# Optimization experiments

Measured on AMD Instinct MI355X. Metric: run time of the kernel, lower is better.

Reference implementation:

```python
import jax, jax.numpy as jnp
import numpy as np

N_TOKENS = 32768
DIM = 2048
N_EXPERTS = 256
N_GROUPS = 8
N_LIMITED_GROUPS = 4
TOP_K = 8
ROUTE_SCALE = 2.5


def setup_inputs() -> dict:
    key = jax.random.key(0)
    k1, k2, k3, k4 = jax.random.split(key, 4)
    x = jax.random.normal(k1, (N_TOKENS, DIM), dtype=jnp.float32)
    w1 = jax.random.normal(k2, (N_EXPERTS, DIM), dtype=jnp.float32) * (DIM ** -0.5)
    b_lin = jax.random.normal(k3, (N_EXPERTS,), dtype=jnp.float32) * 0.02
    bias = jax.random.normal(k4, (N_EXPERTS,), dtype=jnp.float32) * 0.02
    return {"x": x, "w1": w1, "b_lin": b_lin, "bias": bias}


def reference(x, w1, b_lin, bias):
    n = x.shape[0]
    # gate GEMM: [N, dim] x [dim, E] -> [N, E]
    logits = jnp.einsum("nd,ed->ne", x, w1) + b_lin
    # sigmoid scoring with L1 normalization
    s = jax.nn.sigmoid(logits)
    s = s / jnp.sum(s, axis=-1, keepdims=True)
    # routing-correction bias (torch code adds it in place, so it is also in the
    # gathered values via the original_scores alias)
    s = s + bias
    original_scores = s
    # group-limited masking: keep only top n_limited_groups groups (amax score,
    # since use_bias=True)
    g = s.reshape(n, N_GROUPS, N_EXPERTS // N_GROUPS)
    group_scores = jnp.max(g, axis=-1)                      # [N, G]
    _, gidx = jax.lax.top_k(group_scores, N_LIMITED_GROUPS)  # [N, Glim]
    keep = jnp.zeros((n, N_GROUPS), dtype=bool).at[
        jnp.arange(n)[:, None], gidx].set(True)
    masked = jnp.where(keep[:, :, None], g, -jnp.inf).reshape(n, N_EXPERTS)
    # final top-k over masked scores, gather from (bias-added) original scores
    _, indices = jax.lax.top_k(masked, TOP_K)               # [N, k]
    values = jnp.take_along_axis(original_scores, indices, axis=1) * ROUTE_SCALE
    return values.astype(x.dtype), indices
```

## Files before the change

### kernel.cpp

```cpp
#include <hip/hip_runtime.h>
#include <math.h>

#define NTOK   32768
#define DIM    2048
#define NE     256
#define NG     8
#define GSZ    32
#define NLIM   4
#define TOPK   8
#define RSCALE 2.5f
#define TAU    4e-7f

#define BT      64
#define THREADS 256
#define KT      16
#define NKT     (DIM / KT)
#define WOFF    262144
#define TILE_B  16384

typedef __bf16 bf16x8 __attribute__((ext_vector_type(8)));
typedef float  f32x16 __attribute__((ext_vector_type(16)));

typedef const __attribute__((address_space(1))) void GASV;
typedef __attribute__((address_space(3))) void LASV;

__device__ __forceinline__ void gload16(const void* g, void* l) {
    __builtin_amdgcn_global_load_lds((GASV*)g, (LASV*)l, 16, 0, 0);
}

__device__ __forceinline__ void split_pack(float4 a, float4 b,
                                           bf16x8& h8, bf16x8& r8) {
    float v[8] = {a.x, a.y, a.z, a.w, b.x, b.y, b.z, b.w};
    union { unsigned int u[4]; bf16x8 v8; } H, R;
#pragma unroll
    for (int q = 0; q < 4; ++q) {
        const unsigned int u0 = __float_as_uint(v[2 * q]);
        const unsigned int u1 = __float_as_uint(v[2 * q + 1]);
        H.u[q] = (u0 >> 16) | (u1 & 0xFFFF0000u);
        const float r0 = v[2 * q]     - __uint_as_float(u0 & 0xFFFF0000u);
        const float r1 = v[2 * q + 1] - __uint_as_float(u1 & 0xFFFF0000u);
        R.u[q] = (__float_as_uint(r0) >> 16) |
                 (__float_as_uint(r1) & 0xFFFF0000u);
    }
    h8 = H.v8; r8 = R.v8;
}

__global__ __launch_bounds__(256) void wsplit_kernel(
    const float* __restrict__ w1, unsigned int* __restrict__ wt)
{
    const int g  = blockIdx.x * 256 + threadIdx.x;
    const int e  = g & 255;
    const int hi = (g >> 8) & 1;
    const int p  = (g >> 9) & 1;
    const int kt = g >> 10;
    const float* src = w1 + (size_t)e * DIM + kt * 16 + hi * 8;

    uint4 o;
    unsigned int w[4];
#pragma unroll
    for (int q = 0; q < 4; ++q) {
        const float v0 = src[2 * q], v1 = src[2 * q + 1];
        const unsigned int u0 = __float_as_uint(v0);
        const unsigned int u1 = __float_as_uint(v1);
        if (p == 0) {
            w[q] = (u0 >> 16) | (u1 & 0xFFFF0000u);
        } else {
            const float r0 = v0 - __uint_as_float(u0 & 0xFFFF0000u);
            const float r1 = v1 - __uint_as_float(u1 & 0xFFFF0000u);
            w[q] = (__float_as_uint(r0) >> 16) |
                   (__float_as_uint(r1) & 0xFFFF0000u);
        }
    }
    o.x = w[0]; o.y = w[1]; o.z = w[2]; o.w = w[3];
    *(uint4*)(wt + (size_t)g * 4) = o;
}

__global__ __launch_bounds__(THREADS, 3) void router_pass1(
    const float* __restrict__ x, const unsigned int* __restrict__ wt,
    const float* __restrict__ b_lin, const float* __restrict__ bias,
    float* __restrict__ out_vals, float* __restrict__ out_idx,
    int* __restrict__ wsI)
{
    __shared__ union {
        alignas(16) char B[3 * TILE_B];
        float sc[32 * 260];
    } sm;

    const int tid  = threadIdx.x;
    const int lane = tid & 63;
    const int wave = tid >> 6;
    const int l31  = lane & 31;
    const int hi   = lane >> 5;
    const int wm   = wave >> 1;
    const int wn   = wave & 1;
    const int t0   = blockIdx.x * BT;

    const float4* xrow =
        (const float4*)(x + (size_t)(t0 + wm * 32 + l31) * DIM) + hi * 2;

    const char* wsrc = (const char*)wt;

    char* p_cur = sm.B;
    char* p_nxt = sm.B + TILE_B;
    char* p_stg = sm.B + 2 * TILE_B;

    auto STAGE = [&](char* ldsbase, int kt) {
#pragma unroll
        for (int q = 0; q < 4; ++q) {
            const int chunk = wave * 4 + q;
            gload16(wsrc + (size_t)kt * TILE_B + chunk * 1024 + lane * 16,
                    ldsbase + chunk * 1024);
        }
    };

    f32x16 acc[4] = {};

    float4 xa0 = xrow[0], xa1 = xrow[1];
    __builtin_amdgcn_sched_barrier(0);
    STAGE(p_cur, 0);
    __builtin_amdgcn_sched_barrier(0);
    float4 xb0 = xrow[4], xb1 = xrow[5];
    __builtin_amdgcn_sched_barrier(0);
    STAGE(p_nxt, 1);
    __builtin_amdgcn_sched_barrier(0);

    const int e_base = (wn * 128 + l31) * 16;
    const int hi4k   = hi * 4096;

    for (int kt = 0; kt < NKT; ++kt) {
        if (kt < NKT - 1) asm volatile("s_waitcnt vmcnt(6)");
        else              asm volatile("s_waitcnt vmcnt(0)");
        __builtin_amdgcn_sched_barrier(0);
        __builtin_amdgcn_s_barrier();
        __builtin_amdgcn_sched_barrier(0);

        float4 xc0, xc1;
        if (kt + 2 < NKT) {
            xc0 = xrow[(kt + 2) * 4];
            xc1 = xrow[(kt + 2) * 4 + 1];
            __builtin_amdgcn_sched_barrier(0);
            STAGE(p_stg, kt + 2);
            __builtin_amdgcn_sched_barrier(0);
        }

        bf16x8 ah, ar;
        split_pack(xa0, xa1, ah, ar);

        __builtin_amdgcn_s_setprio(1);
#pragma unroll
        for (int j = 0; j < 4; ++j) {
            const int eo = e_base + j * 512;
            bf16x8 bh = *(const bf16x8*)(p_cur + hi4k + eo);
            bf16x8 br = *(const bf16x8*)(p_cur + 8192 + hi4k + eo);
            acc[j] = __builtin_amdgcn_mfma_f32_32x32x16_bf16(ah, bh, acc[j], 0, 0, 0);
            acc[j] = __builtin_amdgcn_mfma_f32_32x32x16_bf16(ah, br, acc[j], 0, 0, 0);
            acc[j] = __builtin_amdgcn_mfma_f32_32x32x16_bf16(ar, bh, acc[j], 0, 0, 0);
        }
        __builtin_amdgcn_s_setprio(0);

        xa0 = xb0; xa1 = xb1; xb0 = xc0; xb1 = xc1;
        char* t = p_cur; p_cur = p_nxt; p_nxt = p_stg; p_stg = t;
    }

    __syncthreads();

    const int tx = tid & 31;
    const int ty = tid >> 5;
    float blv[8], bsv[8];
#pragma unroll
    for (int j = 0; j < 8; ++j) {
        blv[j] = b_lin[tx + 32 * j];
        bsv[j] = bias[tx + 32 * j];
    }

    for (int h = 0; h < 2; ++h) {
        if (h) __syncthreads();
        if (wm == h) {
#pragma unroll
            for (int j = 0; j < 4; ++j) {
#pragma unroll
                for (int r = 0; r < 16; ++r) {
                    const int row = (r & 3) + 8 * (r >> 2) + 4 * hi;
                    const int e   = wn * 128 + j * 32 + l31;
                    sm.sc[row * 260 + e] = acc[j][r];
                }
            }
        }
        __syncthreads();

#pragma unroll
        for (int i = 0; i < 4; ++i) {
            const int row = ty * 4 + i;
            float s8[8];
            float psum = 0.0f;
#pragma unroll
            for (int j = 0; j < 8; ++j) {
                const float lg = sm.sc[row * 260 + tx + 32 * j] + blv[j];
                const float s = 1.0f / (1.0f + expf(-lg));
                s8[j] = s;
                psum += s;
            }
#pragma unroll
            for (int m = 1; m <= 16; m <<= 1) psum += __shfl_xor(psum, m);
#pragma unroll
            for (int j = 0; j < 8; ++j) s8[j] = s8[j] / psum + bsv[j];

            float gm[8];
#pragma unroll
            for (int j = 0; j < 8; ++j) gm[j] = s8[j];
#pragma unroll
            for (int m = 1; m <= 16; m <<= 1)
#pragma unroll
                for (int j = 0; j < 8; ++j)
                    gm[j] = fmaxf(gm[j], __shfl_xor(gm[j], m));

            unsigned keep = 0u;
            float g4v = 0.0f, g5v = 0.0f;
#pragma unroll
            for (int r = 0; r < 5; ++r) {
                float bv = -1e30f; int bg = 0;
#pragma unroll
                for (int g = 0; g < 8; ++g)
                    if (!((keep >> g) & 1) && gm[g] > bv) { bv = gm[g]; bg = g; }
                if (r < 4) { keep |= 1u << bg; g4v = bv; }
                else g5v = bv;
            }
            float margin = g4v - g5v;

#pragma unroll
            for (int j = 0; j < 8; ++j)
                if (!((keep >> j) & 1)) s8[j] = -1e30f;

            float tv[9]; int te[9];
#pragma unroll
            for (int r = 0; r < 9; ++r) {
                float bv = -1e30f; int bj = 8;
#pragma unroll
                for (int j = 0; j < 8; ++j)
                    if (s8[j] > bv) { bv = s8[j]; bj = j; }
                int be = (bj < 8) ? (tx + 32 * bj) : 9999;
#pragma unroll
                for (int m = 1; m <= 16; m <<= 1) {
                    const float ov = __shfl_xor(bv, m);
                    const int   oe = __shfl_xor(be, m);
                    if (ov > bv || (ov == bv && oe < be)) { bv = ov; be = oe; }
                }
                tv[r] = bv; te[r] = be;
                if (r < 8 && (be & 31) == tx) s8[be >> 5] = -1e30f;
            }
#pragma unroll
            for (int r = 0; r < 8; ++r) margin = fminf(margin, tv[r] - tv[r + 1]);

            if (tx == 0) {
                const int t = t0 + h * 32 + row;
                const int base = t * TOPK;
#pragma unroll
                for (int r = 0; r < 8; ++r) {
                    out_vals[base + r] = tv[r] * RSCALE;
                    out_idx[base + r]  = (float)te[r];
                }
                if (margin < TAU) {
                    const int slot = atomicAdd(&wsI[0], 1);
                    if (slot < 60000) wsI[4 + slot] = t;
                }
            }
        }
    }
}

__global__ __launch_bounds__(THREADS, 1) void router_pass2(
    const float* __restrict__ x, const float* __restrict__ w1,
    const float* __restrict__ b_lin, const float* __restrict__ bias,
    float* __restrict__ out_vals, float* __restrict__ out_idx,
    const int* __restrict__ wsI)
{
    __shared__ double xrow[DIM];
    __shared__ double red[256];
    __shared__ double sc[NE];

    const int tid = threadIdx.x;
    const int count = min(wsI[0], 60000);
    const int* list = wsI + 4;
    const float4* x4 = (const float4*)x;
    const float4* w4 = (const float4*)w1;

    for (int li = blockIdx.x; li < count; li += gridDim.x) {
        const int t = list[li];
        __syncthreads();
#pragma unroll
        for (int q = 0; q < 2; ++q) {
            const int id = tid + 256 * q;
            const float4 v = x4[t * 512 + id];
            xrow[id * 4 + 0] = (double)v.x;
            xrow[id * 4 + 1] = (double)v.y;
            xrow[id * 4 + 2] = (double)v.z;
            xrow[id * 4 + 3] = (double)v.w;
        }
        __syncthreads();

        const int e = tid;
        double a0 = 0.0, a1 = 0.0, a2 = 0.0, a3 = 0.0;
#pragma unroll 2
        for (int k4 = 0; k4 < 512; k4 += 4) {
#pragma unroll
            for (int z = 0; z < 4; ++z) {
                const float4 wv = w4[e * 512 + k4 + z];
                double* ac = (z == 0) ? &a0 : (z == 1) ? &a1 : (z == 2) ? &a2 : &a3;
                *ac = fma(xrow[(k4 + z) * 4 + 0], (double)wv.x, *ac);
                *ac = fma(xrow[(k4 + z) * 4 + 1], (double)wv.y, *ac);
                *ac = fma(xrow[(k4 + z) * 4 + 2], (double)wv.z, *ac);
                *ac = fma(xrow[(k4 + z) * 4 + 3], (double)wv.w, *ac);
            }
        }
        const double lg = ((a0 + a1) + (a2 + a3)) + (double)b_lin[e];
        const double s = 1.0 / (1.0 + exp(-lg));
        red[tid] = s;
        __syncthreads();
        for (int off = 128; off > 0; off >>= 1) {
            if (tid < off) red[tid] += red[tid + off];
            __syncthreads();
        }
        sc[e] = s / red[0] + (double)bias[e];
        __syncthreads();

        if (tid == 0) {
            double gmax[NG];
            for (int g = 0; g < NG; ++g) {
                double mx = -INFINITY;
                for (int q = 0; q < GSZ; ++q) {
                    const double v = sc[g * GSZ + q];
                    mx = (v > mx) ? v : mx;
                }
                gmax[g] = mx;
            }
            unsigned keep = 0u;
            for (int r = 0; r < NLIM; ++r) {
                int best = 0; double bv = -INFINITY;
                for (int g = 0; g < NG; ++g) {
                    if (keep & (1u << g)) continue;
                    if (gmax[g] > bv) { bv = gmax[g]; best = g; }
                }
                keep |= 1u << best;
            }
            double tv[TOPK]; int ti[TOPK];
            for (int r = 0; r < TOPK; ++r) { tv[r] = -INFINITY; ti[r] = NE; }
            for (int g = 0; g < NG; ++g) {
                if (!(keep & (1u << g))) continue;
                for (int q = 0; q < GSZ; ++q) {
                    const int ee = g * GSZ + q;
                    const double v = sc[ee];
                    if (v > tv[TOPK - 1]) {
                        int p = TOPK - 1;
                        while (p > 0 && v > tv[p - 1]) {
                            tv[p] = tv[p - 1]; ti[p] = ti[p - 1]; --p;
                        }
                        tv[p] = v; ti[p] = ee;
                    }
                }
            }
            const int base = t * TOPK;
            for (int r = 0; r < TOPK; ++r) {
                out_vals[base + r] = (float)(tv[r] * (double)RSCALE);
                out_idx[base + r]  = (float)ti[r];
            }
        }
    }
}

extern "C" void kernel_launch(void* const* d_in, const int* in_sizes, int n_in,
                              void* d_out, int out_size, void* d_ws, size_t ws_size,
                              hipStream_t stream) {
    const float* x     = (const float*)d_in[0];
    const float* w1    = (const float*)d_in[1];
    const float* b_lin = (const float*)d_in[2];
    const float* bias  = (const float*)d_in[3];
    float* out_vals = (float*)d_out;
    float* out_idx  = (float*)d_out + (size_t)NTOK * TOPK;

    int* wsI = (int*)d_ws;
    unsigned int* wt = (unsigned int*)((char*)d_ws + WOFF);

    hipMemsetAsync(d_ws, 0, 16, stream);
    wsplit_kernel<<<dim3(512), 256, 0, stream>>>(w1, wt);
    router_pass1<<<dim3(NTOK / BT), THREADS, 0, stream>>>(
        x, wt, b_lin, bias, out_vals, out_idx, wsI);
    router_pass2<<<dim3(256), THREADS, 0, stream>>>(
        x, w1, b_lin, bias, out_vals, out_idx, (const int*)d_ws);
}
```

Before: 268.4 us.

## Stage x tiles through LDS with coalesced loads instead of per-lane row loads

```diff
diff --git a/kernel.cpp b/kernel.cpp
--- a/kernel.cpp
+++ b/kernel.cpp
@@ -26,23 +26,6 @@
 
 __device__ __forceinline__ void gload16(const void* g, void* l) {
     __builtin_amdgcn_global_load_lds((GASV*)g, (LASV*)l, 16, 0, 0);
-}
-
-__device__ __forceinline__ void split_pack(float4 a, float4 b,
-                                           bf16x8& h8, bf16x8& r8) {
-    float v[8] = {a.x, a.y, a.z, a.w, b.x, b.y, b.z, b.w};
-    union { unsigned int u[4]; bf16x8 v8; } H, R;
-#pragma unroll
-    for (int q = 0; q < 4; ++q) {
-        const unsigned int u0 = __float_as_uint(v[2 * q]);
-        const unsigned int u1 = __float_as_uint(v[2 * q + 1]);
-        H.u[q] = (u0 >> 16) | (u1 & 0xFFFF0000u);
-        const float r0 = v[2 * q]     - __uint_as_float(u0 & 0xFFFF0000u);
-        const float r1 = v[2 * q + 1] - __uint_as_float(u1 & 0xFFFF0000u);
-        R.u[q] = (__float_as_uint(r0) >> 16) |
-                 (__float_as_uint(r1) & 0xFFFF0000u);
-    }
-    h8 = H.v8; r8 = R.v8;
 }
 
 __global__ __launch_bounds__(256) void wsplit_kernel(
@@ -75,14 +58,17 @@
     *(uint4*)(wt + (size_t)g * 4) = o;
 }
 
-__global__ __launch_bounds__(THREADS, 3) void router_pass1(
+__global__ __launch_bounds__(THREADS, 2) void router_pass1(
     const float* __restrict__ x, const unsigned int* __restrict__ wt,
     const float* __restrict__ b_lin, const float* __restrict__ bias,
     float* __restrict__ out_vals, float* __restrict__ out_idx,
     int* __restrict__ wsI)
 {
     __shared__ union {
-        alignas(16) char B[3 * TILE_B];
+        struct {
+            alignas(16) char B[3 * TILE_B];
+            float xs[2][16][72];
+        } t;
         float sc[32 * 260];
     } sm;
 
@@ -95,14 +81,14 @@
     const int wn   = wave & 1;
     const int t0   = blockIdx.x * BT;
 
-    const float4* xrow =
-        (const float4*)(x + (size_t)(t0 + wm * 32 + l31) * DIM) + hi * 2;
+    const int xtr = tid >> 2, xkq = tid & 3;
+    const float* xgp = x + (size_t)(t0 + xtr) * DIM + xkq * 4;
+    const int acol = wm * 32 + l31;
 
     const char* wsrc = (const char*)wt;
-
-    char* p_cur = sm.B;
-    char* p_nxt = sm.B + TILE_B;
-    char* p_stg = sm.B + 2 * TILE_B;
+    char* bc = sm.t.B;
+    char* bn = sm.t.B + TILE_B;
+    char* bs = sm.t.B + 2 * TILE_B;
 
     auto STAGE = [&](char* ldsbase, int kt) {
 #pragma unroll
@@ -112,55 +98,85 @@
                     ldsbase + chunk * 1024);
         }
     };
+    auto XWRITE = [&](int b, float4 v) {
+        sm.t.xs[b][xkq * 4 + 0][xtr] = v.x;
+        sm.t.xs[b][xkq * 4 + 1][xtr] = v.y;
+        sm.t.xs[b][xkq * 4 + 2][xtr] = v.z;
+        sm.t.xs[b][xkq * 4 + 3][xtr] = v.w;
+    };
+    auto AFRAG = [&](int b, bf16x8& ah, bf16x8& ar) {
+        union { unsigned int u[4]; bf16x8 v; } H, R;
+#pragma unroll
+        for (int q = 0; q < 4; ++q) {
+            const float f0 = sm.t.xs[b][hi * 8 + 2 * q][acol];
+            const float f1 = sm.t.xs[b][hi * 8 + 2 * q + 1][acol];
+            const unsigned int u0 = __float_as_uint(f0);
+            const unsigned int u1 = __float_as_uint(f1);
+            H.u[q] = (u0 >> 16) | (u1 & 0xFFFF0000u);
+            const float r0 = f0 - __uint_as_float(u0 & 0xFFFF0000u);
+            const float r1 = f1 - __uint_as_float(u1 & 0xFFFF0000u);
+            R.u[q] = (__float_as_uint(r0) >> 16) |
+                     (__float_as_uint(r1) & 0xFFFF0000u);
+        }
+        ah = H.v; ar = R.v;
+    };
 
     f32x16 acc[4] = {};
-
-    float4 xa0 = xrow[0], xa1 = xrow[1];
-    __builtin_amdgcn_sched_barrier(0);
-    STAGE(p_cur, 0);
-    __builtin_amdgcn_sched_barrier(0);
-    float4 xb0 = xrow[4], xb1 = xrow[5];
-    __builtin_amdgcn_sched_barrier(0);
-    STAGE(p_nxt, 1);
-    __builtin_amdgcn_sched_barrier(0);
-
     const int e_base = (wn * 128 + l31) * 16;
     const int hi4k   = hi * 4096;
 
-    for (int kt = 0; kt < NKT; ++kt) {
-        if (kt < NKT - 1) asm volatile("s_waitcnt vmcnt(6)");
-        else              asm volatile("s_waitcnt vmcnt(0)");
+    float4 rA, rB;
+
+    rA = *(const float4*)xgp;
+    __builtin_amdgcn_sched_barrier(0);
+    STAGE(bc, 0);
+    __builtin_amdgcn_sched_barrier(0);
+    rB = *(const float4*)(xgp + KT);
+    __builtin_amdgcn_sched_barrier(0);
+    STAGE(bn, 1);
+    __builtin_amdgcn_sched_barrier(0);
+    asm volatile("s_waitcnt vmcnt(9)");
+    __builtin_amdgcn_sched_barrier(0);
+    XWRITE(0, rA);
+
+    auto ITER = [&](int kt, float4 wrv, float4& ldv, bool last) {
+        if (!last) asm volatile("s_waitcnt vmcnt(4)");
+        else       asm volatile("s_waitcnt vmcnt(0)");
+        __builtin_amdgcn_sched_barrier(0);
+        asm volatile("s_waitcnt lgkmcnt(0)");
         __builtin_amdgcn_sched_barrier(0);
         __builtin_amdgcn_s_barrier();
         __builtin_amdgcn_sched_barrier(0);
-
-        float4 xc0, xc1;
-        if (kt + 2 < NKT) {
-            xc0 = xrow[(kt + 2) * 4];
-            xc1 = xrow[(kt + 2) * 4 + 1];
-            __builtin_amdgcn_sched_barrier(0);
-            STAGE(p_stg, kt + 2);
-            __builtin_amdgcn_sched_barrier(0);
-        }
+        if (kt + 1 < NKT) XWRITE((kt + 1) & 1, wrv);
+        if (kt + 2 < NKT) ldv = *(const float4*)(xgp + (kt + 2) * KT);
+        __builtin_amdgcn_sched_barrier(0);
+        if (kt + 2 < NKT) STAGE(bs, kt + 2);
+        __builtin_amdgcn_sched_barrier(0);
 
         bf16x8 ah, ar;
-        split_pack(xa0, xa1, ah, ar);
-
+        AFRAG(kt & 1, ah, ar);
         __builtin_amdgcn_s_setprio(1);
 #pragma unroll
         for (int j = 0; j < 4; ++j) {
             const int eo = e_base + j * 512;
-            bf16x8 bh = *(const bf16x8*)(p_cur + hi4k + eo);
-            bf16x8 br = *(const bf16x8*)(p_cur + 8192 + hi4k + eo);
+            bf16x8 bh = *(const bf16x8*)(bc + hi4k + eo);
+            bf16x8 br = *(const bf16x8*)(bc + 8192 + hi4k + eo);
             acc[j] = __builtin_amdgcn_mfma_f32_32x32x16_bf16(ah, bh, acc[j], 0, 0, 0);
             acc[j] = __builtin_amdgcn_mfma_f32_32x32x16_bf16(ah, br, acc[j], 0, 0, 0);
             acc[j] = __builtin_amdgcn_mfma_f32_32x32x16_bf16(ar, bh, acc[j], 0, 0, 0);
         }
         __builtin_amdgcn_s_setprio(0);
-
-        xa0 = xb0; xa1 = xb1; xb0 = xc0; xb1 = xc1;
-        char* t = p_cur; p_cur = p_nxt; p_nxt = p_stg; p_stg = t;
+        char* t = bc; bc = bn; bn = bs; bs = t;
+    };
+
+    for (int kt2 = 0; kt2 < NKT - 4; kt2 += 2) {
+        ITER(kt2,     rB, rA, false);
+        ITER(kt2 + 1, rA, rB, false);
     }
+    ITER(NKT - 4, rB, rA, false);
+    ITER(NKT - 3, rA, rB, false);
+    ITER(NKT - 2, rB, rA, false);
+    ITER(NKT - 1, rA, rB, true);
 
     __syncthreads();
 
```

New measurement: 261.2 us. 1.03x faster.

## Shrink token tile to 32 and stage split x operand through LDS

Applied to the files above, without the earlier changes.

```diff
diff --git a/kernel.cpp b/kernel.cpp
--- a/kernel.cpp
+++ b/kernel.cpp
@@ -11,7 +11,7 @@
 #define RSCALE 2.5f
 #define TAU    4e-7f
 
-#define BT      64
+#define BT      32
 #define THREADS 256
 #define KT      16
 #define NKT     (DIM / KT)
@@ -26,23 +26,6 @@
 
 __device__ __forceinline__ void gload16(const void* g, void* l) {
     __builtin_amdgcn_global_load_lds((GASV*)g, (LASV*)l, 16, 0, 0);
-}
-
-__device__ __forceinline__ void split_pack(float4 a, float4 b,
-                                           bf16x8& h8, bf16x8& r8) {
-    float v[8] = {a.x, a.y, a.z, a.w, b.x, b.y, b.z, b.w};
-    union { unsigned int u[4]; bf16x8 v8; } H, R;
-#pragma unroll
-    for (int q = 0; q < 4; ++q) {
-        const unsigned int u0 = __float_as_uint(v[2 * q]);
-        const unsigned int u1 = __float_as_uint(v[2 * q + 1]);
-        H.u[q] = (u0 >> 16) | (u1 & 0xFFFF0000u);
-        const float r0 = v[2 * q]     - __uint_as_float(u0 & 0xFFFF0000u);
-        const float r1 = v[2 * q + 1] - __uint_as_float(u1 & 0xFFFF0000u);
-        R.u[q] = (__float_as_uint(r0) >> 16) |
-                 (__float_as_uint(r1) & 0xFFFF0000u);
-    }
-    h8 = H.v8; r8 = R.v8;
 }
 
 __global__ __launch_bounds__(256) void wsplit_kernel(
@@ -75,94 +58,93 @@
     *(uint4*)(wt + (size_t)g * 4) = o;
 }
 
-__global__ __launch_bounds__(THREADS, 3) void router_pass1(
+__global__ __launch_bounds__(THREADS, 4) void router_pass1(
     const float* __restrict__ x, const unsigned int* __restrict__ wt,
     const float* __restrict__ b_lin, const float* __restrict__ bias,
     float* __restrict__ out_vals, float* __restrict__ out_idx,
     int* __restrict__ wsI)
 {
     __shared__ union {
-        alignas(16) char B[3 * TILE_B];
+        struct {
+            alignas(16) char B[2][TILE_B];
+            unsigned short xs[2][2][32][16];
+        } t;
         float sc[32 * 260];
     } sm;
 
     const int tid  = threadIdx.x;
     const int lane = tid & 63;
-    const int wave = tid >> 6;
+    const int wn   = tid >> 6;
     const int l31  = lane & 31;
     const int hi   = lane >> 5;
-    const int wm   = wave >> 1;
-    const int wn   = wave & 1;
     const int t0   = blockIdx.x * BT;
 
-    const float4* xrow =
-        (const float4*)(x + (size_t)(t0 + wm * 32 + l31) * DIM) + hi * 2;
+    const int xtok = tid >> 3, xk2 = tid & 7;
+    const float2* xg = (const float2*)(x + (size_t)(t0 + xtok) * DIM) + xk2;
 
     const char* wsrc = (const char*)wt;
 
-    char* p_cur = sm.B;
-    char* p_nxt = sm.B + TILE_B;
-    char* p_stg = sm.B + 2 * TILE_B;
-
     auto STAGE = [&](char* ldsbase, int kt) {
 #pragma unroll
         for (int q = 0; q < 4; ++q) {
-            const int chunk = wave * 4 + q;
+            const int chunk = wn * 4 + q;
             gload16(wsrc + (size_t)kt * TILE_B + chunk * 1024 + lane * 16,
                     ldsbase + chunk * 1024);
         }
     };
-
-    f32x16 acc[4] = {};
-
-    float4 xa0 = xrow[0], xa1 = xrow[1];
+    auto XWRITE = [&](int b, float2 v) {
+        const unsigned int u0 = __float_as_uint(v.x);
+        const unsigned int u1 = __float_as_uint(v.y);
+        const unsigned int hp = (u0 >> 16) | (u1 & 0xFFFF0000u);
+        const float r0 = v.x - __uint_as_float(u0 & 0xFFFF0000u);
+        const float r1 = v.y - __uint_as_float(u1 & 0xFFFF0000u);
+        const unsigned int rp = (__float_as_uint(r0) >> 16) |
+                                (__float_as_uint(r1) & 0xFFFF0000u);
+        *(unsigned int*)&sm.t.xs[b][0][xtok][xk2 * 2] = hp;
+        *(unsigned int*)&sm.t.xs[b][1][xtok][xk2 * 2] = rp;
+    };
+
+    f32x16 acc[2] = {};
+
+    float2 xv = xg[0];
     __builtin_amdgcn_sched_barrier(0);
-    STAGE(p_cur, 0);
+    STAGE(sm.t.B[0], 0);
     __builtin_amdgcn_sched_barrier(0);
-    float4 xb0 = xrow[4], xb1 = xrow[5];
+    asm volatile("s_waitcnt vmcnt(4)");
     __builtin_amdgcn_sched_barrier(0);
-    STAGE(p_nxt, 1);
-    __builtin_amdgcn_sched_barrier(0);
-
-    const int e_base = (wn * 128 + l31) * 16;
-    const int hi4k   = hi * 4096;
+    XWRITE(0, xv);
+    __syncthreads();
 
     for (int kt = 0; kt < NKT; ++kt) {
-        if (kt < NKT - 1) asm volatile("s_waitcnt vmcnt(6)");
-        else              asm volatile("s_waitcnt vmcnt(0)");
-        __builtin_amdgcn_sched_barrier(0);
-        __builtin_amdgcn_s_barrier();
-        __builtin_amdgcn_sched_barrier(0);
-
-        float4 xc0, xc1;
-        if (kt + 2 < NKT) {
-            xc0 = xrow[(kt + 2) * 4];
-            xc1 = xrow[(kt + 2) * 4 + 1];
+        const int cur = kt & 1, nxt = cur ^ 1;
+        if (kt + 1 < NKT) {
+            xv = xg[(kt + 1) * 8];
             __builtin_amdgcn_sched_barrier(0);
-            STAGE(p_stg, kt + 2);
+            STAGE(sm.t.B[nxt], kt + 1);
             __builtin_amdgcn_sched_barrier(0);
         }
 
-        bf16x8 ah, ar;
-        split_pack(xa0, xa1, ah, ar);
-
-        __builtin_amdgcn_s_setprio(1);
-#pragma unroll
-        for (int j = 0; j < 4; ++j) {
-            const int eo = e_base + j * 512;
-            bf16x8 bh = *(const bf16x8*)(p_cur + hi4k + eo);
-            bf16x8 br = *(const bf16x8*)(p_cur + 8192 + hi4k + eo);
-            acc[j] = __builtin_amdgcn_mfma_f32_32x32x16_bf16(ah, bh, acc[j], 0, 0, 0);
-            acc[j] = __builtin_amdgcn_mfma_f32_32x32x16_bf16(ah, br, acc[j], 0, 0, 0);
-            acc[j] = __builtin_amdgcn_mfma_f32_32x32x16_bf16(ar, bh, acc[j], 0, 0, 0);
-        }
-        __builtin_amdgcn_s_setprio(0);
-
-        xa0 = xb0; xa1 = xb1; xb0 = xc0; xb1 = xc1;
-        char* t = p_cur; p_cur = p_nxt; p_nxt = p_stg; p_stg = t;
-    }
-
-    __syncthreads();
+        bf16x8 ah = *(const bf16x8*)&sm.t.xs[cur][0][l31][hi * 8];
+        bf16x8 ar = *(const bf16x8*)&sm.t.xs[cur][1][l31][hi * 8];
+#pragma unroll
+        for (int ni = 0; ni < 2; ++ni) {
+            const int e = wn * 64 + ni * 32 + l31;
+            const char* pb = sm.t.B[cur] + ((0 * 2 + hi) * 256 + e) * 16;
+            const char* pr = sm.t.B[cur] + ((1 * 2 + hi) * 256 + e) * 16;
+            bf16x8 bh = *(const bf16x8*)pb;
+            bf16x8 br = *(const bf16x8*)pr;
+            acc[ni] = __builtin_amdgcn_mfma_f32_32x32x16_bf16(ah, bh, acc[ni], 0, 0, 0);
+            acc[ni] = __builtin_amdgcn_mfma_f32_32x32x16_bf16(ah, br, acc[ni], 0, 0, 0);
+            acc[ni] = __builtin_amdgcn_mfma_f32_32x32x16_bf16(ar, bh, acc[ni], 0, 0, 0);
+        }
+
+        if (kt + 1 < NKT) {
+            asm volatile("s_waitcnt vmcnt(4)");
+            __builtin_amdgcn_sched_barrier(0);
+            XWRITE(nxt, xv);
+        }
+        __syncthreads();
+    }
 
     const int tx = tid & 31;
     const int ty = tid >> 5;
@@ -173,102 +155,97 @@
         bsv[j] = bias[tx + 32 * j];
     }
 
-    for (int h = 0; h < 2; ++h) {
-        if (h) __syncthreads();
-        if (wm == h) {
-#pragma unroll
-            for (int j = 0; j < 4; ++j) {
-#pragma unroll
-                for (int r = 0; r < 16; ++r) {
-                    const int row = (r & 3) + 8 * (r >> 2) + 4 * hi;
-                    const int e   = wn * 128 + j * 32 + l31;
-                    sm.sc[row * 260 + e] = acc[j][r];
-                }
-            }
-        }
-        __syncthreads();
-
-#pragma unroll
-        for (int i = 0; i < 4; ++i) {
-            const int row = ty * 4 + i;
-            float s8[8];
-            float psum = 0.0f;
-#pragma unroll
-            for (int j = 0; j < 8; ++j) {
-                const float lg = sm.sc[row * 260 + tx + 32 * j] + blv[j];
-                const float s = 1.0f / (1.0f + expf(-lg));
-                s8[j] = s;
-                psum += s;
-            }
-#pragma unroll
-            for (int m = 1; m <= 16; m <<= 1) psum += __shfl_xor(psum, m);
-#pragma unroll
-            for (int j = 0; j < 8; ++j) s8[j] = s8[j] / psum + bsv[j];
-
-            float gm[8];
-#pragma unroll
-            for (int j = 0; j < 8; ++j) gm[j] = s8[j];
-#pragma unroll
-            for (int m = 1; m <= 16; m <<= 1)
-#pragma unroll
-                for (int j = 0; j < 8; ++j)
-                    gm[j] = fmaxf(gm[j], __shfl_xor(gm[j], m));
-
-            unsigned keep = 0u;
-            float g4v = 0.0f, g5v = 0.0f;
-#pragma unroll
-            for (int r = 0; r < 5; ++r) {
-                float bv = -1e30f; int bg = 0;
-#pragma unroll
-                for (int g = 0; g < 8; ++g)
-                    if (!((keep >> g) & 1) && gm[g] > bv) { bv = gm[g]; bg = g; }
-                if (r < 4) { keep |= 1u << bg; g4v = bv; }
-                else g5v = bv;
-            }
-            float margin = g4v - g5v;
-
+#pragma unroll
+    for (int ni = 0; ni < 2; ++ni) {
+#pragma unroll
+        for (int r = 0; r < 16; ++r) {
+            const int row = (r & 3) + 8 * (r >> 2) + 4 * hi;
+            const int e   = wn * 64 + ni * 32 + l31;
+            sm.sc[row * 260 + e] = acc[ni][r];
+        }
+    }
+    __syncthreads();
+
+#pragma unroll
+    for (int i = 0; i < 4; ++i) {
+        const int row = ty * 4 + i;
+        float s8[8];
+        float psum = 0.0f;
+#pragma unroll
+        for (int j = 0; j < 8; ++j) {
+            const float lg = sm.sc[row * 260 + tx + 32 * j] + blv[j];
+            const float s = 1.0f / (1.0f + expf(-lg));
+            s8[j] = s;
+            psum += s;
+        }
+#pragma unroll
+        for (int m = 1; m <= 16; m <<= 1) psum += __shfl_xor(psum, m);
+#pragma unroll
+        for (int j = 0; j < 8; ++j) s8[j] = s8[j] / psum + bsv[j];
+
+        float gm[8];
+#pragma unroll
+        for (int j = 0; j < 8; ++j) gm[j] = s8[j];
+#pragma unroll
+        for (int m = 1; m <= 16; m <<= 1)
 #pragma unroll
             for (int j = 0; j < 8; ++j)
-                if (!((keep >> j) & 1)) s8[j] = -1e30f;
-
-            float tv[9]; int te[9];
-#pragma unroll
-            for (int r = 0; r < 9; ++r) {
-                float bv = -1e30f; int bj = 8;
-#pragma unroll
-                for (int j = 0; j < 8; ++j)
-                    if (s8[j] > bv) { bv = s8[j]; bj = j; }
-                int be = (bj < 8) ? (tx + 32 * bj) : 9999;
-#pragma unroll
-                for (int m = 1; m <= 16; m <<= 1) {
-                    const float ov = __shfl_xor(bv, m);
-                    const int   oe = __shfl_xor(be, m);
-                    if (ov > bv || (ov == bv && oe < be)) { bv = ov; be = oe; }
-                }
-                tv[r] = bv; te[r] = be;
-                if (r < 8 && (be & 31) == tx) s8[be >> 5] = -1e30f;
-            }
-#pragma unroll
-            for (int r = 0; r < 8; ++r) margin = fminf(margin, tv[r] - tv[r + 1]);
-
-            if (tx == 0) {
-                const int t = t0 + h * 32 + row;
-                const int base = t * TOPK;
-#pragma unroll
-                for (int r = 0; r < 8; ++r) {
-                    out_vals[base + r] = tv[r] * RSCALE;
-                    out_idx[base + r]  = (float)te[r];
-                }
-                if (margin < TAU) {
-                    const int slot = atomicAdd(&wsI[0], 1);
-                    if (slot < 60000) wsI[4 + slot] = t;
-                }
-            }
-        }
-    }
-}
-
-__global__ __launch_bounds__(THREADS, 1) void router_pass2(
+                gm[j] = fmaxf(gm[j], __shfl_xor(gm[j], m));
+
+        unsigned keep = 0u;
+        float g4v = 0.0f, g5v = 0.0f;
+#pragma unroll
+        for (int r = 0; r < 5; ++r) {
+            float bv = -1e30f; int bg = 0;
+#pragma unroll
+            for (int g = 0; g < 8; ++g)
+                if (!((keep >> g) & 1) && gm[g] > bv) { bv = gm[g]; bg = g; }
+            if (r < 4) { keep |= 1u << bg; g4v = bv; }
+            else g5v = bv;
+        }
+        float margin = g4v - g5v;
+
+#pragma unroll
+        for (int j = 0; j < 8; ++j)
+            if (!((keep >> j) & 1)) s8[j] = -1e30f;
+
+        float tv[9]; int te[9];
+#pragma unroll
+        for (int r = 0; r < 9; ++r) {
+            float bv = -1e30f; int bj = 8;
+#pragma unroll
+            for (int j = 0; j < 8; ++j)
+                if (s8[j] > bv) { bv = s8[j]; bj = j; }
+            int be = (bj < 8) ? (tx + 32 * bj) : 9999;
+#pragma unroll
+            for (int m = 1; m <= 16; m <<= 1) {
+                const float ov = __shfl_xor(bv, m);
+                const int   oe = __shfl_xor(be, m);
+                if (ov > bv || (ov == bv && oe < be)) { bv = ov; be = oe; }
+            }
+            tv[r] = bv; te[r] = be;
+            if (r < 8 && (be & 31) == tx) s8[be >> 5] = -1e30f;
+        }
+#pragma unroll
+        for (int r = 0; r < 8; ++r) margin = fminf(margin, tv[r] - tv[r + 1]);
+
+        if (tx == 0) {
+            const int t = t0 + row;
+            const int base = t * TOPK;
+#pragma unroll
+            for (int r = 0; r < 8; ++r) {
+                out_vals[base + r] = tv[r] * RSCALE;
+                out_idx[base + r]  = (float)te[r];
+            }
+            if (margin < TAU) {
+                const int slot = atomicAdd(&wsI[0], 1);
+                if (slot < 60000) wsI[4 + slot] = t;
+            }
+        }
+    }
+}
+
+__global__ __launch_bounds__(256, 1) void router_pass2(
     const float* __restrict__ x, const float* __restrict__ w1,
     const float* __restrict__ b_lin, const float* __restrict__ bias,
     float* __restrict__ out_vals, float* __restrict__ out_idx,
@@ -384,6 +361,6 @@
     wsplit_kernel<<<dim3(512), 256, 0, stream>>>(w1, wt);
     router_pass1<<<dim3(NTOK / BT), THREADS, 0, stream>>>(
         x, wt, b_lin, bias, out_vals, out_idx, wsI);
-    router_pass2<<<dim3(256), THREADS, 0, stream>>>(
+    router_pass2<<<dim3(256), 256, 0, stream>>>(
         x, w1, b_lin, bias, out_vals, out_idx, (const int*)d_ws);
 }
```

Result: no change. 269.7 us (+0.5%).
